# Kernel tuning notes

Measured on AMD Instinct MI355X. Metric: run time of the kernel, lower is better.

The kernel has to match this reference:

```python
import jax
jax.config.update("jax_enable_x64", True)
import jax.numpy as jnp
import numpy as np

SIGMA_2 = 0.1  # SNR = 10 dB -> sigma^2 = 1/10^(10/10)
P = 1.0        # total transmit power

NT, NR, DK, KU, BR = 64, 4, 2, 8, 16
BATCH = 256


def setup_inputs() -> dict:
    key = jax.random.key(0)
    k1, k2 = jax.random.split(key)
    channel = jax.random.normal(k1, (BATCH, NT * NR * BR * 2 * KU), dtype=jnp.float32)
    pred_w = 2 * NR * DK * KU * BR + DK * DK * KU * BR  # 2560
    prediction = jax.random.normal(k2, (BATCH, pred_w), dtype=jnp.float32)
    return {"channel": channel, "prediction": prediction,
            "Nt": NT, "Nr": NR, "dk": DK, "K": KU, "B": BR}


def reference(channel, prediction, Nt, Nr, dk, K, B):
    # --- unpack complex channel: [b, Nt, Nr, B, 2K] -> [b, Nr, Nt, B, K] complex
    Hc = channel.reshape(-1, Nt, Nr, B, 2 * K).astype(jnp.complex128)
    H = Hc[..., :K] + 1j * Hc[..., K:]
    H = jnp.transpose(H, (0, 2, 1, 3, 4))  # [b, Nr, Nt, B, K]

    nu = 2 * Nr * dk * K * B
    u_flat = prediction[:, :nu]
    w_flat = prediction[:, nu:nu + dk * dk * K * B]
    Uc = u_flat.reshape(-1, Nr, dk, B, 2 * K).astype(jnp.complex128)
    U = Uc[..., :K] + 1j * Uc[..., K:]           # [b, Nr, dk, B, K]
    W = w_flat.reshape(-1, dk, dk, B, K).astype(jnp.complex128)  # real-valued W

    # HHU[b,:,:,f,k] = H^H U  -> [b, Nt, dk, B, K]
    HHU = jnp.einsum('brtfk,brdfk->btdfk', jnp.conj(H), U)

    # sum over (rb, user) of sigma2/p * trace(U W U^H)
    tr_UWU = (SIGMA_2 / P) * jnp.einsum('brdfk,bdefk,brefk->b', U, W, jnp.conj(U))
    # sum over (rb, user) of (H^H U) W (H^H U)^H  -> [b, Nt, Nt]
    quad = jnp.einsum('btdfk,bdefk,bsefk->bts', HHU, W, jnp.conj(HHU))
    temp_B = quad + tr_UWU[:, None, None] * jnp.eye(Nt, dtype=jnp.complex128)
    temp_B_inv = jnp.linalg.inv(temp_B)  # batched Nt x Nt complex inverse

    # HUW[b,:,:,k] = sum_rb (H^H U) W  -> [b, Nt, dk, K]
    HUW = jnp.einsum('btdfk,bdefk->btek', HHU, W)
    V0 = jnp.einsum('bts,bsdk->btdk', temp_B_inv, HUW)  # [b, Nt, dk, K]

    # l2-normalize flattened precoder per sample (tf.linalg.normalize)
    flat = V0.reshape(-1, Nt * dk * K)
    flat = flat / jnp.linalg.norm(flat, axis=1, keepdims=True)
    V0 = flat.reshape(-1, Nt, dk, K)

    # power normalization: trace(sum_k V_k V_k^H)
    trace_VV = jnp.einsum('btdk,btdk->b', V0, jnp.conj(V0))
    scale = jnp.sqrt(P / jnp.real(trace_VV).astype(jnp.float32))
    V = V0 * scale.astype(jnp.complex128)[:, None, None, None]

    V = V.reshape(-1, Nt, dk, K, 1)
    return jnp.concatenate([jnp.real(V), jnp.imag(V)], axis=4).astype(jnp.float32)
```

## Files before the change

### kernel.cpp

```cpp
#include <hip/hip_runtime.h>
#include <math.h>


#define SAUG 84
#define STP  65

namespace {
union alignas(16) ShU {
    struct { float4 TtP[2][2][8][STP]; float4 HtP[2][2][8][STP]; } p1;
    float2 Aug[64][SAUG];
};
union alignas(16) ShV {
    struct { float2 U[4 * 258]; float W[512]; } in;
    float2 xout[64][17];
};
}

__device__ __forceinline__ float2 cmul(float2 x, float2 y) {
    return make_float2(x.x * y.x - x.y * y.y, x.x * y.y + x.y * y.x);
}

__global__ __launch_bounds__(512, 1)
void uw2v_kernel(const float* __restrict__ channel,
                 const float* __restrict__ prediction,
                 float2* __restrict__ out)
{
    __shared__ ShU sh;
    __shared__ ShV sv;
    __shared__ alignas(16) float2 prow[2][80];
    __shared__ float2 redbuf[8];
    __shared__ float  fred[8];

    const int b   = blockIdx.x;
    const int tid = threadIdx.x;
    const int wv  = tid >> 6;
    const float* pred = prediction + (size_t)b * 2560;
    const float* chan = channel + (size_t)b * 65536;

    #pragma unroll
    for (int i = 0; i < 2; ++i) {
        int m = tid + i * 512;
        int r = m >> 8, d = (m >> 7) & 1, f = (m >> 3) & 15, k = m & 7;
        const float* src = pred + (((r * 2 + d) * 16 + f) << 4);
        sv.in.U[r * 258 + ((d * 16 + f) << 3) + k] = make_float2(src[k], src[k + 8]);
    }
    sv.in.W[tid] = pred[2048 + tid];
    __syncthreads();

    const int half = tid >> 8;
    const int lt   = tid & 255;
    const int t4 = lt >> 2, r4 = lt & 3;
    const int a  = lt >> 4, bb = lt & 15;
    const int bit0 = r4 & 1, bit1 = (r4 >> 1) & 1;
    const int kkb  = 4 * bit0 + 2 * bit1;
    const int mpb  = kkb >> 1;
    const int fbase = half << 3;
    const int tr_r = lt >> 5, tr_d = (lt >> 4) & 1, tr_e = (lt >> 3) & 1, tr_k = lt & 7;

    float2 accA[4][4], accB[4][4];
    #pragma unroll
    for (int i = 0; i < 4; ++i)
        #pragma unroll
        for (int j = 0; j < 4; ++j) {
            accA[i][j] = make_float2(0.f, 0.f);
            accB[i][j] = make_float2(0.f, 0.f);
        }
    float2 huw[4] = {make_float2(0,0), make_float2(0,0), make_float2(0,0), make_float2(0,0)};
    float2 tracc  = make_float2(0.f, 0.f);

    const float* hbase = chan + ((t4 * 4 + r4) << 8) + (fbase << 4);

    #pragma unroll 1
    for (int fi = 0; fi < 8; ++fi) {
        const int f = fbase + fi;
        const float4 ca = *(const float4*)(hbase + (fi << 4) + 0);
        const float4 cb = *(const float4*)(hbase + (fi << 4) + 4);
        const float4 ci = *(const float4*)(hbase + (fi << 4) + 8);
        const float4 cd = *(const float4*)(hbase + (fi << 4) + 12);

        const float4* U0p = (const float4*)&sv.in.U[r4 * 258 + (f << 3)];
        const float4* U1p = (const float4*)&sv.in.U[r4 * 258 + ((16 + f) << 3)];
        const float4 u0q0 = U0p[0], u0q1 = U0p[1], u0q2 = U0p[2], u0q3 = U0p[3];
        const float4 u1q0 = U1p[0], u1q1 = U1p[1], u1q2 = U1p[2], u1q3 = U1p[3];

        float2 val0[8], val1[8];
        #define MK2(K, HR, HI, U0R, U0I, U1R, U1I) \
            val0[K] = make_float2((HR)*(U0R) + (HI)*(U0I), (HR)*(U0I) - (HI)*(U0R)); \
            val1[K] = make_float2((HR)*(U1R) + (HI)*(U1I), (HR)*(U1I) - (HI)*(U1R));
        MK2(0, ca.x, ci.x, u0q0.x, u0q0.y, u1q0.x, u1q0.y)
        MK2(1, ca.y, ci.y, u0q0.z, u0q0.w, u1q0.z, u1q0.w)
        MK2(2, ca.z, ci.z, u0q1.x, u0q1.y, u1q1.x, u1q1.y)
        MK2(3, ca.w, ci.w, u0q1.z, u0q1.w, u1q1.z, u1q1.w)
        MK2(4, cb.x, cd.x, u0q2.x, u0q2.y, u1q2.x, u1q2.y)
        MK2(5, cb.y, cd.y, u0q2.z, u0q2.w, u1q2.z, u1q2.w)
        MK2(6, cb.z, cd.z, u0q3.x, u0q3.y, u1q3.x, u1q3.y)
        MK2(7, cb.w, cd.w, u0q3.z, u0q3.w, u1q3.z, u1q3.w)
        #undef MK2

        float2 s1d0[4], s1d1[4];
        #pragma unroll
        for (int q = 0; q < 4; ++q) {
            float2 k0 = bit0 ? val0[4 + q] : val0[q];
            float2 n0 = bit0 ? val0[q]     : val0[4 + q];
            float2 k1 = bit0 ? val1[4 + q] : val1[q];
            float2 n1 = bit0 ? val1[q]     : val1[4 + q];
            n0.x = __shfl_xor(n0.x, 1); n0.y = __shfl_xor(n0.y, 1);
            n1.x = __shfl_xor(n1.x, 1); n1.y = __shfl_xor(n1.y, 1);
            s1d0[q] = make_float2(k0.x + n0.x, k0.y + n0.y);
            s1d1[q] = make_float2(k1.x + n1.x, k1.y + n1.y);
        }
        float2 h0[2], h1[2];
        #pragma unroll
        for (int jj = 0; jj < 2; ++jj) {
            float2 k0 = bit1 ? s1d0[2 + jj] : s1d0[jj];
            float2 n0 = bit1 ? s1d0[jj]     : s1d0[2 + jj];
            float2 k1 = bit1 ? s1d1[2 + jj] : s1d1[jj];
            float2 n1 = bit1 ? s1d1[jj]     : s1d1[2 + jj];
            n0.x = __shfl_xor(n0.x, 2); n0.y = __shfl_xor(n0.y, 2);
            n1.x = __shfl_xor(n1.x, 2); n1.y = __shfl_xor(n1.y, 2);
            h0[jj] = make_float2(k0.x + n0.x, k0.y + n0.y);
            h1[jj] = make_float2(k1.x + n1.x, k1.y + n1.y);
        }

        if (lt < 128) {
            float w   = sv.in.W[((tr_d * 2 + tr_e) * 16 + f) * 8 + tr_k];
            float2 u1 = sv.in.U[tr_r * 258 + ((tr_d * 16 + f) << 3) + tr_k];
            float2 u2 = sv.in.U[tr_r * 258 + ((tr_e * 16 + f) << 3) + tr_k];
            tracc.x += w * (u1.x * u2.x + u1.y * u2.y);
            tracc.y += w * (u1.y * u2.x - u1.x * u2.y);
        }

        const int p = fi & 1;
        #pragma unroll
        for (int e = 0; e < 2; ++e) {
            float w0a = sv.in.W[(e * 16 + f) * 8 + kkb];
            float w0b = sv.in.W[(e * 16 + f) * 8 + kkb + 1];
            float w1a = sv.in.W[((2 + e) * 16 + f) * 8 + kkb];
            float w1b = sv.in.W[((2 + e) * 16 + f) * 8 + kkb + 1];
            float2 tva = make_float2(h0[0].x * w0a + h1[0].x * w1a,
                                     h0[0].y * w0a + h1[0].y * w1a);
            float2 tvb = make_float2(h0[1].x * w0b + h1[1].x * w1b,
                                     h0[1].y * w0b + h1[1].y * w1b);
            sh.p1.TtP[p][half][e * 4 + mpb][t4] = make_float4(tva.x, tva.y, tvb.x, tvb.y);
            huw[e * 2 + 0].x += tva.x; huw[e * 2 + 0].y += tva.y;
            huw[e * 2 + 1].x += tvb.x; huw[e * 2 + 1].y += tvb.y;
        }
        sh.p1.HtP[p][half][mpb][t4]     = make_float4(h0[0].x, h0[0].y, h0[1].x, h0[1].y);
        sh.p1.HtP[p][half][4 + mpb][t4] = make_float4(h1[0].x, h1[0].y, h1[1].x, h1[1].y);
        __syncthreads();

        #pragma unroll
        for (int mp = 0; mp < 8; ++mp) {
            float4 tq[4], hq[4];
            #pragma unroll
            for (int i = 0; i < 4; ++i) tq[i] = sh.p1.TtP[p][half][mp][a + 16 * i];
            #pragma unroll
            for (int j = 0; j < 4; ++j) hq[j] = sh.p1.HtP[p][half][mp][bb + 16 * j];
            #pragma unroll
            for (int i = 0; i < 4; ++i)
                #pragma unroll
                for (int j = 0; j < 4; ++j) {
                    float2 va = accA[i][j], vb = accB[i][j];
                    va.x = fmaf(tq[i].x, hq[j].x, va.x);
                    va.y = fmaf(tq[i].x, hq[j].y, va.y);
                    vb.x = fmaf(tq[i].y, hq[j].x, vb.x);
                    vb.y = fmaf(tq[i].y, hq[j].y, vb.y);
                    va.x = fmaf(tq[i].z, hq[j].z, va.x);
                    va.y = fmaf(tq[i].z, hq[j].w, va.y);
                    vb.x = fmaf(tq[i].w, hq[j].z, vb.x);
                    vb.y = fmaf(tq[i].w, hq[j].w, vb.y);
                    accA[i][j] = va; accB[i][j] = vb;
                }
        }
    }

    #pragma unroll
    for (int off = 32; off; off >>= 1) {
        tracc.x += __shfl_xor(tracc.x, off);
        tracc.y += __shfl_xor(tracc.y, off);
    }
    if ((tid & 63) == 0) redbuf[wv] = tracc;
    __syncthreads();
    float2 trv = make_float2(0.f, 0.f);
    #pragma unroll
    for (int w = 0; w < 8; ++w) { trv.x += redbuf[w].x; trv.y += redbuf[w].y; }
    trv.x *= 0.1f; trv.y *= 0.1f;

    if (half == 0) {
        #pragma unroll
        for (int i = 0; i < 4; ++i)
            #pragma unroll
            for (int j = 0; j < 4; ++j) {
                float2 v = make_float2(accA[i][j].x + accB[i][j].y,
                                       accB[i][j].x - accA[i][j].y);
                int row = a + 16 * i, col = bb + 16 * j;
                if (row == col) { v.x += trv.x; v.y += trv.y; }
                sh.Aug[row][col] = v;
            }
        #pragma unroll
        for (int e = 0; e < 2; ++e)
            #pragma unroll
            for (int jj = 0; jj < 2; ++jj)
                sh.Aug[t4][64 + e * 8 + kkb + jj] = huw[e * 2 + jj];
    }
    __syncthreads();
    if (half == 1) {
        #pragma unroll
        for (int i = 0; i < 4; ++i)
            #pragma unroll
            for (int j = 0; j < 4; ++j) {
                int row = a + 16 * i, col = bb + 16 * j;
                float2 v = sh.Aug[row][col];
                v.x += accA[i][j].x + accB[i][j].y;
                v.y += accB[i][j].x - accA[i][j].y;
                sh.Aug[row][col] = v;
            }
        #pragma unroll
        for (int e = 0; e < 2; ++e)
            #pragma unroll
            for (int jj = 0; jj < 2; ++jj) {
                int col = 64 + e * 8 + kkb + jj;
                float2 v = sh.Aug[t4][col];
                v.x += huw[e * 2 + jj].x; v.y += huw[e * 2 + jj].y;
                sh.Aug[t4][col] = v;
            }
    }
    __syncthreads();

    const int gi = tid >> 3, gc = tid & 7;
    const int colbase = 10 * gc;
    const int lanebase = (tid & 63) & 56;

    float2 xr[10];
    {
        const float4* rp = (const float4*)&sh.Aug[gi][colbase];
        float4 q0 = rp[0], q1 = rp[1], q2 = rp[2], q3 = rp[3], q4 = rp[4];
        xr[0] = make_float2(q0.x, q0.y); xr[1] = make_float2(q0.z, q0.w);
        xr[2] = make_float2(q1.x, q1.y); xr[3] = make_float2(q1.z, q1.w);
        xr[4] = make_float2(q2.x, q2.y); xr[5] = make_float2(q2.z, q2.w);
        xr[6] = make_float2(q3.x, q3.y); xr[7] = make_float2(q3.z, q3.w);
        xr[8] = make_float2(q4.x, q4.y); xr[9] = make_float2(q4.z, q4.w);
    }
    if (gi == 0) {
        float4* wp = (float4*)&prow[0][colbase];
        wp[0] = make_float4(xr[0].x, xr[0].y, xr[1].x, xr[1].y);
        wp[1] = make_float4(xr[2].x, xr[2].y, xr[3].x, xr[3].y);
        wp[2] = make_float4(xr[4].x, xr[4].y, xr[5].x, xr[5].y);
        wp[3] = make_float4(xr[6].x, xr[6].y, xr[7].x, xr[7].y);
        wp[4] = make_float4(xr[8].x, xr[8].y, xr[9].x, xr[9].y);
    }
    __syncthreads();

    float2 myipv = make_float2(0.f, 0.f);

    #pragma unroll 1
    for (int ks = 0; ks < 64; ++ks) {
        const int pb = ks & 1;
        const float4* pp = (const float4*)&prow[pb][colbase];
        float4 p0 = pp[0], p1 = pp[1], p2 = pp[2], p3 = pp[3], p4 = pp[4];
        float2 pr[10];
        pr[0] = make_float2(p0.x, p0.y); pr[1] = make_float2(p0.z, p0.w);
        pr[2] = make_float2(p1.x, p1.y); pr[3] = make_float2(p1.z, p1.w);
        pr[4] = make_float2(p2.x, p2.y); pr[5] = make_float2(p2.z, p2.w);
        pr[6] = make_float2(p3.x, p3.y); pr[7] = make_float2(p3.z, p3.w);
        pr[8] = make_float2(p4.x, p4.y); pr[9] = make_float2(p4.z, p4.w);

        float2 z = prow[pb][ks];
        float  zi = 1.0f / (z.x * z.x + z.y * z.y);
        float2 ipv = make_float2(z.x * zi, -z.y * zi);

        float2 cand = make_float2(0.f, 0.f);
        #pragma unroll
        for (int c = 0; c < 10; ++c)
            if (colbase + c == ks) cand = xr[c];
        int srcl = lanebase + (ks / 10);
        float2 Lv;
        Lv.x = __shfl(cand.x, srcl);
        Lv.y = __shfl(cand.y, srcl);

        if (gi == ks) {
            myipv = ipv;
        } else {
            float2 L = cmul(Lv, ipv);
            #pragma unroll
            for (int c = 0; c < 10; ++c) {
                xr[c].x -= L.x * pr[c].x - L.y * pr[c].y;
                xr[c].y -= L.x * pr[c].y + L.y * pr[c].x;
            }
        }
        if (gi == ks + 1) {
            float4* wp = (float4*)&prow[pb ^ 1][colbase];
            wp[0] = make_float4(xr[0].x, xr[0].y, xr[1].x, xr[1].y);
            wp[1] = make_float4(xr[2].x, xr[2].y, xr[3].x, xr[3].y);
            wp[2] = make_float4(xr[4].x, xr[4].y, xr[5].x, xr[5].y);
            wp[3] = make_float4(xr[6].x, xr[6].y, xr[7].x, xr[7].y);
            wp[4] = make_float4(xr[8].x, xr[8].y, xr[9].x, xr[9].y);
        }
        __syncthreads();
    }

    float ss = 0.f;
    if (gc == 6) {
        #pragma unroll
        for (int c = 4; c < 10; ++c) {
            float2 xv = cmul(xr[c], myipv);
            ss += xv.x * xv.x + xv.y * xv.y;
            sv.xout[gi][c - 4] = xv;
        }
    } else if (gc == 7) {
        #pragma unroll
        for (int c = 0; c < 10; ++c) {
            float2 xv = cmul(xr[c], myipv);
            ss += xv.x * xv.x + xv.y * xv.y;
            sv.xout[gi][6 + c] = xv;
        }
    }
    #pragma unroll
    for (int off = 32; off; off >>= 1) ss += __shfl_xor(ss, off);
    if ((tid & 63) == 0) fred[wv] = ss;
    __syncthreads();
    float total = 0.f;
    #pragma unroll
    for (int w = 0; w < 8; ++w) total += fred[w];
    float invn = rsqrtf(total);
    #pragma unroll
    for (int q = 0; q < 2; ++q) {
        int m = tid + q * 512;
        float2 v = sv.xout[m >> 4][m & 15];
        out[(size_t)b * 1024 + m] = make_float2(v.x * invn, v.y * invn);
    }
}

extern "C" void kernel_launch(void* const* d_in, const int* in_sizes, int n_in,
                              void* d_out, int out_size, void* d_ws, size_t ws_size,
                              hipStream_t stream) {
    const float* channel    = (const float*)d_in[0];
    const float* prediction = (const float*)d_in[1];
    int batch = in_sizes[0] / 65536;
    uw2v_kernel<<<dim3(batch), dim3(512), 0, stream>>>(channel, prediction,
                                                       (float2*)d_out);
}
```

Baseline: 169.6 us.

## Double block to 1024 threads, split subcarriers across four groups

The block grows from 512 to 1024 threads. The Gram accumulation now splits the 16 resource blocks across four thread groups of 4 each instead of two groups of 8, which halves the serial loop length. The partial sums are reduced through two augmented shared matrices, and the diagonal regularizer is applied while summing them. The Gauss-Jordan elimination now gives each thread 5 columns instead of 10, which shortens the per-step work. The cost is doubled shared staging, more threads per block (which limits registers per thread), and 64 block-wide barriers over more waves.

```diff
diff --git a/kernel.cpp b/kernel.cpp
--- a/kernel.cpp
+++ b/kernel.cpp
@@ -7,8 +7,8 @@
 
 namespace {
 union alignas(16) ShU {
-    struct { float4 TtP[2][2][8][STP]; float4 HtP[2][2][8][STP]; } p1;
-    float2 Aug[64][SAUG];
+    struct { float4 TtP[2][4][8][STP]; float4 HtP[2][4][8][STP]; } p1;
+    struct { float2 A[64][SAUG]; float2 B[64][SAUG]; } aug;
 };
 union alignas(16) ShV {
     struct { float2 U[4 * 258]; float W[512]; } in;
@@ -20,7 +20,7 @@
     return make_float2(x.x * y.x - x.y * y.y, x.x * y.y + x.y * y.x);
 }
 
-__global__ __launch_bounds__(512, 1)
+__global__ __launch_bounds__(1024)
 void uw2v_kernel(const float* __restrict__ channel,
                  const float* __restrict__ prediction,
                  float2* __restrict__ out)
@@ -28,8 +28,8 @@
     __shared__ ShU sh;
     __shared__ ShV sv;
     __shared__ alignas(16) float2 prow[2][80];
-    __shared__ float2 redbuf[8];
-    __shared__ float  fred[8];
+    __shared__ float2 redbuf[16];
+    __shared__ float  fred[16];
 
     const int b   = blockIdx.x;
     const int tid = threadIdx.x;
@@ -37,24 +37,23 @@
     const float* pred = prediction + (size_t)b * 2560;
     const float* chan = channel + (size_t)b * 65536;
 
-    #pragma unroll
-    for (int i = 0; i < 2; ++i) {
-        int m = tid + i * 512;
+    {
+        int m = tid;
         int r = m >> 8, d = (m >> 7) & 1, f = (m >> 3) & 15, k = m & 7;
         const float* src = pred + (((r * 2 + d) * 16 + f) << 4);
         sv.in.U[r * 258 + ((d * 16 + f) << 3) + k] = make_float2(src[k], src[k + 8]);
     }
-    sv.in.W[tid] = pred[2048 + tid];
-    __syncthreads();
-
-    const int half = tid >> 8;
-    const int lt   = tid & 255;
+    if (tid < 512) sv.in.W[tid] = pred[2048 + tid];
+    __syncthreads();
+
+    const int grp = tid >> 8;
+    const int lt  = tid & 255;
     const int t4 = lt >> 2, r4 = lt & 3;
     const int a  = lt >> 4, bb = lt & 15;
     const int bit0 = r4 & 1, bit1 = (r4 >> 1) & 1;
     const int kkb  = 4 * bit0 + 2 * bit1;
     const int mpb  = kkb >> 1;
-    const int fbase = half << 3;
+    const int fbase = grp << 2;
     const int tr_r = lt >> 5, tr_d = (lt >> 4) & 1, tr_e = (lt >> 3) & 1, tr_k = lt & 7;
 
     float2 accA[4][4], accB[4][4];
@@ -71,7 +70,7 @@
     const float* hbase = chan + ((t4 * 4 + r4) << 8) + (fbase << 4);
 
     #pragma unroll 1
-    for (int fi = 0; fi < 8; ++fi) {
+    for (int fi = 0; fi < 4; ++fi) {
         const int f = fbase + fi;
         const float4 ca = *(const float4*)(hbase + (fi << 4) + 0);
         const float4 cb = *(const float4*)(hbase + (fi << 4) + 4);
@@ -141,21 +140,21 @@
                                      h0[0].y * w0a + h1[0].y * w1a);
             float2 tvb = make_float2(h0[1].x * w0b + h1[1].x * w1b,
                                      h0[1].y * w0b + h1[1].y * w1b);
-            sh.p1.TtP[p][half][e * 4 + mpb][t4] = make_float4(tva.x, tva.y, tvb.x, tvb.y);
+            sh.p1.TtP[p][grp][e * 4 + mpb][t4] = make_float4(tva.x, tva.y, tvb.x, tvb.y);
             huw[e * 2 + 0].x += tva.x; huw[e * 2 + 0].y += tva.y;
             huw[e * 2 + 1].x += tvb.x; huw[e * 2 + 1].y += tvb.y;
         }
-        sh.p1.HtP[p][half][mpb][t4]     = make_float4(h0[0].x, h0[0].y, h0[1].x, h0[1].y);
-        sh.p1.HtP[p][half][4 + mpb][t4] = make_float4(h1[0].x, h1[0].y, h1[1].x, h1[1].y);
+        sh.p1.HtP[p][grp][mpb][t4]     = make_float4(h0[0].x, h0[0].y, h0[1].x, h0[1].y);
+        sh.p1.HtP[p][grp][4 + mpb][t4] = make_float4(h1[0].x, h1[0].y, h1[1].x, h1[1].y);
         __syncthreads();
 
         #pragma unroll
         for (int mp = 0; mp < 8; ++mp) {
             float4 tq[4], hq[4];
             #pragma unroll
-            for (int i = 0; i < 4; ++i) tq[i] = sh.p1.TtP[p][half][mp][a + 16 * i];
-            #pragma unroll
-            for (int j = 0; j < 4; ++j) hq[j] = sh.p1.HtP[p][half][mp][bb + 16 * j];
+            for (int i = 0; i < 4; ++i) tq[i] = sh.p1.TtP[p][grp][mp][a + 16 * i];
+            #pragma unroll
+            for (int j = 0; j < 4; ++j) hq[j] = sh.p1.HtP[p][grp][mp][bb + 16 * j];
             #pragma unroll
             for (int i = 0; i < 4; ++i)
                 #pragma unroll
@@ -183,71 +182,65 @@
     __syncthreads();
     float2 trv = make_float2(0.f, 0.f);
     #pragma unroll
-    for (int w = 0; w < 8; ++w) { trv.x += redbuf[w].x; trv.y += redbuf[w].y; }
+    for (int w = 0; w < 16; ++w) { trv.x += redbuf[w].x; trv.y += redbuf[w].y; }
     trv.x *= 0.1f; trv.y *= 0.1f;
 
-    if (half == 0) {
+    if ((grp & 1) == 0) {
+        float2 (*Dst)[SAUG] = (grp == 0) ? sh.aug.A : sh.aug.B;
         #pragma unroll
         for (int i = 0; i < 4; ++i)
             #pragma unroll
             for (int j = 0; j < 4; ++j) {
-                float2 v = make_float2(accA[i][j].x + accB[i][j].y,
-                                       accB[i][j].x - accA[i][j].y);
-                int row = a + 16 * i, col = bb + 16 * j;
-                if (row == col) { v.x += trv.x; v.y += trv.y; }
-                sh.Aug[row][col] = v;
+                Dst[a + 16 * i][bb + 16 * j] =
+                    make_float2(accA[i][j].x + accB[i][j].y,
+                                accB[i][j].x - accA[i][j].y);
             }
         #pragma unroll
         for (int e = 0; e < 2; ++e)
             #pragma unroll
             for (int jj = 0; jj < 2; ++jj)
-                sh.Aug[t4][64 + e * 8 + kkb + jj] = huw[e * 2 + jj];
-    }
-    __syncthreads();
-    if (half == 1) {
+                Dst[t4][64 + e * 8 + kkb + jj] = huw[e * 2 + jj];
+    }
+    __syncthreads();
+    if (grp & 1) {
+        float2 (*Dst)[SAUG] = (grp == 1) ? sh.aug.A : sh.aug.B;
         #pragma unroll
         for (int i = 0; i < 4; ++i)
             #pragma unroll
             for (int j = 0; j < 4; ++j) {
-                int row = a + 16 * i, col = bb + 16 * j;
-                float2 v = sh.Aug[row][col];
+                float2 v = Dst[a + 16 * i][bb + 16 * j];
                 v.x += accA[i][j].x + accB[i][j].y;
                 v.y += accB[i][j].x - accA[i][j].y;
-                sh.Aug[row][col] = v;
+                Dst[a + 16 * i][bb + 16 * j] = v;
             }
         #pragma unroll
         for (int e = 0; e < 2; ++e)
             #pragma unroll
             for (int jj = 0; jj < 2; ++jj) {
                 int col = 64 + e * 8 + kkb + jj;
-                float2 v = sh.Aug[t4][col];
+                float2 v = Dst[t4][col];
                 v.x += huw[e * 2 + jj].x; v.y += huw[e * 2 + jj].y;
-                sh.Aug[t4][col] = v;
-            }
-    }
-    __syncthreads();
-
-    const int gi = tid >> 3, gc = tid & 7;
-    const int colbase = 10 * gc;
-    const int lanebase = (tid & 63) & 56;
-
-    float2 xr[10];
-    {
-        const float4* rp = (const float4*)&sh.Aug[gi][colbase];
-        float4 q0 = rp[0], q1 = rp[1], q2 = rp[2], q3 = rp[3], q4 = rp[4];
-        xr[0] = make_float2(q0.x, q0.y); xr[1] = make_float2(q0.z, q0.w);
-        xr[2] = make_float2(q1.x, q1.y); xr[3] = make_float2(q1.z, q1.w);
-        xr[4] = make_float2(q2.x, q2.y); xr[5] = make_float2(q2.z, q2.w);
-        xr[6] = make_float2(q3.x, q3.y); xr[7] = make_float2(q3.z, q3.w);
-        xr[8] = make_float2(q4.x, q4.y); xr[9] = make_float2(q4.z, q4.w);
+                Dst[t4][col] = v;
+            }
+    }
+    __syncthreads();
+
+    const int gi = tid >> 4, gc = tid & 15;
+    const int cb = gc * 5;
+    const int lanebase = (tid & 63) & 48;
+
+    float2 xr[5];
+    #pragma unroll
+    for (int c = 0; c < 5; ++c) {
+        float2 v = sh.aug.A[gi][cb + c];
+        float2 w = sh.aug.B[gi][cb + c];
+        v.x += w.x; v.y += w.y;
+        if (gi == cb + c) { v.x += trv.x; v.y += trv.y; }
+        xr[c] = v;
     }
     if (gi == 0) {
-        float4* wp = (float4*)&prow[0][colbase];
-        wp[0] = make_float4(xr[0].x, xr[0].y, xr[1].x, xr[1].y);
-        wp[1] = make_float4(xr[2].x, xr[2].y, xr[3].x, xr[3].y);
-        wp[2] = make_float4(xr[4].x, xr[4].y, xr[5].x, xr[5].y);
-        wp[3] = make_float4(xr[6].x, xr[6].y, xr[7].x, xr[7].y);
-        wp[4] = make_float4(xr[8].x, xr[8].y, xr[9].x, xr[9].y);
+        #pragma unroll
+        for (int c = 0; c < 5; ++c) prow[0][cb + c] = xr[c];
     }
     __syncthreads();
 
@@ -256,14 +249,9 @@
     #pragma unroll 1
     for (int ks = 0; ks < 64; ++ks) {
         const int pb = ks & 1;
-        const float4* pp = (const float4*)&prow[pb][colbase];
-        float4 p0 = pp[0], p1 = pp[1], p2 = pp[2], p3 = pp[3], p4 = pp[4];
-        float2 pr[10];
-        pr[0] = make_float2(p0.x, p0.y); pr[1] = make_float2(p0.z, p0.w);
-        pr[2] = make_float2(p1.x, p1.y); pr[3] = make_float2(p1.z, p1.w);
-        pr[4] = make_float2(p2.x, p2.y); pr[5] = make_float2(p2.z, p2.w);
-        pr[6] = make_float2(p3.x, p3.y); pr[7] = make_float2(p3.z, p3.w);
-        pr[8] = make_float2(p4.x, p4.y); pr[9] = make_float2(p4.z, p4.w);
+        float2 pr[5];
+        #pragma unroll
+        for (int c = 0; c < 5; ++c) pr[c] = prow[pb][cb + c];
 
         float2 z = prow[pb][ks];
         float  zi = 1.0f / (z.x * z.x + z.y * z.y);
@@ -271,9 +259,9 @@
 
         float2 cand = make_float2(0.f, 0.f);
         #pragma unroll
-        for (int c = 0; c < 10; ++c)
-            if (colbase + c == ks) cand = xr[c];
-        int srcl = lanebase + (ks / 10);
+        for (int c = 0; c < 5; ++c)
+            if (cb + c == ks) cand = xr[c];
+        int srcl = lanebase + (ks / 5);
         float2 Lv;
         Lv.x = __shfl(cand.x, srcl);
         Lv.y = __shfl(cand.y, srcl);
@@ -283,36 +271,28 @@
         } else {
             float2 L = cmul(Lv, ipv);
             #pragma unroll
-            for (int c = 0; c < 10; ++c) {
+            for (int c = 0; c < 5; ++c) {
                 xr[c].x -= L.x * pr[c].x - L.y * pr[c].y;
                 xr[c].y -= L.x * pr[c].y + L.y * pr[c].x;
             }
         }
         if (gi == ks + 1) {
-            float4* wp = (float4*)&prow[pb ^ 1][colbase];
-            wp[0] = make_float4(xr[0].x, xr[0].y, xr[1].x, xr[1].y);
-            wp[1] = make_float4(xr[2].x, xr[2].y, xr[3].x, xr[3].y);
-            wp[2] = make_float4(xr[4].x, xr[4].y, xr[5].x, xr[5].y);
-            wp[3] = make_float4(xr[6].x, xr[6].y, xr[7].x, xr[7].y);
-            wp[4] = make_float4(xr[8].x, xr[8].y, xr[9].x, xr[9].y);
+            #pragma unroll
+            for (int c = 0; c < 5; ++c) prow[pb ^ 1][cb + c] = xr[c];
         }
         __syncthreads();
     }
 
     float ss = 0.f;
-    if (gc == 6) {
-        #pragma unroll
-        for (int c = 4; c < 10; ++c) {
-            float2 xv = cmul(xr[c], myipv);
-            ss += xv.x * xv.x + xv.y * xv.y;
-            sv.xout[gi][c - 4] = xv;
-        }
-    } else if (gc == 7) {
-        #pragma unroll
-        for (int c = 0; c < 10; ++c) {
-            float2 xv = cmul(xr[c], myipv);
-            ss += xv.x * xv.x + xv.y * xv.y;
-            sv.xout[gi][6 + c] = xv;
+    if (gc >= 12) {
+        #pragma unroll
+        for (int c = 0; c < 5; ++c) {
+            int col = cb + c;
+            if (col >= 64) {
+                float2 xv = cmul(xr[c], myipv);
+                ss += xv.x * xv.x + xv.y * xv.y;
+                sv.xout[gi][col - 64] = xv;
+            }
         }
     }
     #pragma unroll
@@ -321,13 +301,11 @@
     __syncthreads();
     float total = 0.f;
     #pragma unroll
-    for (int w = 0; w < 8; ++w) total += fred[w];
+    for (int w = 0; w < 16; ++w) total += fred[w];
     float invn = rsqrtf(total);
-    #pragma unroll
-    for (int q = 0; q < 2; ++q) {
-        int m = tid + q * 512;
-        float2 v = sv.xout[m >> 4][m & 15];
-        out[(size_t)b * 1024 + m] = make_float2(v.x * invn, v.y * invn);
+    {
+        float2 v = sv.xout[tid >> 4][tid & 15];
+        out[(size_t)b * 1024 + tid] = make_float2(v.x * invn, v.y * invn);
     }
 }
 
@@ -337,6 +315,6 @@
     const float* channel    = (const float*)d_in[0];
     const float* prediction = (const float*)d_in[1];
     int batch = in_sizes[0] / 65536;
-    uw2v_kernel<<<dim3(batch), dim3(512), 0, stream>>>(channel, prediction,
-                                                       (float2*)d_out);
+    uw2v_kernel<<<dim3(batch), dim3(1024), 0, stream>>>(channel, prediction,
+                                                        (float2*)d_out);
 }
```

After: 249.7 us. +47.2%, slower.

## Block Gauss-Jordan elimination into 8-row panels with in-wave cascade and shuffles

Applied to the files above, without the earlier changes.

Restructures the 64-step Gauss-Jordan inversion so each wave holds 8 pivot rows and eliminates them internally with warp shuffles. The other waves then apply the whole panel of 8 pivots read from shared memory. This cuts the block-wide barriers from 64 to about 9 and overlaps the next panel's cascade with the current elimination. The cost is extra shuffle traffic and serialized per-wave cascade work, which sits on the critical path.

```diff
diff --git a/kernel.cpp b/kernel.cpp
--- a/kernel.cpp
+++ b/kernel.cpp
@@ -27,7 +27,8 @@
 {
     __shared__ ShU sh;
     __shared__ ShV sv;
-    __shared__ alignas(16) float2 prow[2][80];
+    __shared__ alignas(16) float2 pivR[2][8][80];
+    __shared__ float2 pivI[2][8];
     __shared__ float2 redbuf[8];
     __shared__ float  fred[8];
 
@@ -228,12 +229,12 @@
     __syncthreads();
 
     const int gi = tid >> 3, gc = tid & 7;
-    const int colbase = 10 * gc;
+    const int cb = 10 * gc;
     const int lanebase = (tid & 63) & 56;
 
     float2 xr[10];
     {
-        const float4* rp = (const float4*)&sh.Aug[gi][colbase];
+        const float4* rp = (const float4*)&sh.Aug[gi][cb];
         float4 q0 = rp[0], q1 = rp[1], q2 = rp[2], q3 = rp[3], q4 = rp[4];
         xr[0] = make_float2(q0.x, q0.y); xr[1] = make_float2(q0.z, q0.w);
         xr[2] = make_float2(q1.x, q1.y); xr[3] = make_float2(q1.z, q1.w);
@@ -241,62 +242,93 @@
         xr[6] = make_float2(q3.x, q3.y); xr[7] = make_float2(q3.z, q3.w);
         xr[8] = make_float2(q4.x, q4.y); xr[9] = make_float2(q4.z, q4.w);
     }
-    if (gi == 0) {
-        float4* wp = (float4*)&prow[0][colbase];
+
+    float2 myipv = make_float2(0.f, 0.f);
+
+    auto cascade = [&](int chunk, int nb) {
+        #pragma unroll
+        for (int p = 0; p < 8; ++p) {
+            const int col = 8 * chunk + p;
+            const int cs  = col / 10;
+            float2 cand = make_float2(0.f, 0.f);
+            #pragma unroll
+            for (int c = 0; c < 10; ++c)
+                if (cb + c == col) cand = xr[c];
+            float2 z, Lv;
+            z.x  = __shfl(cand.x, p * 8 + cs);
+            z.y  = __shfl(cand.y, p * 8 + cs);
+            Lv.x = __shfl(cand.x, lanebase + cs);
+            Lv.y = __shfl(cand.y, lanebase + cs);
+            float  zi  = 1.0f / (z.x * z.x + z.y * z.y);
+            float2 ipv = make_float2(z.x * zi, -z.y * zi);
+            const bool isPiv = (gi == col);
+            if (isPiv) myipv = ipv;
+            float2 pr[10];
+            #pragma unroll
+            for (int c = 0; c < 10; ++c) {
+                pr[c].x = __shfl(xr[c].x, p * 8 + gc);
+                pr[c].y = __shfl(xr[c].y, p * 8 + gc);
+            }
+            if (!isPiv) {
+                float2 L = cmul(Lv, ipv);
+                #pragma unroll
+                for (int c = 0; c < 10; ++c) {
+                    xr[c].x -= L.x * pr[c].x - L.y * pr[c].y;
+                    xr[c].y -= L.x * pr[c].y + L.y * pr[c].x;
+                }
+            }
+        }
+        const int prw = gi & 7;
+        float4* wp = (float4*)&pivR[nb][prw][cb];
         wp[0] = make_float4(xr[0].x, xr[0].y, xr[1].x, xr[1].y);
         wp[1] = make_float4(xr[2].x, xr[2].y, xr[3].x, xr[3].y);
         wp[2] = make_float4(xr[4].x, xr[4].y, xr[5].x, xr[5].y);
         wp[3] = make_float4(xr[6].x, xr[6].y, xr[7].x, xr[7].y);
         wp[4] = make_float4(xr[8].x, xr[8].y, xr[9].x, xr[9].y);
-    }
-    __syncthreads();
-
-    float2 myipv = make_float2(0.f, 0.f);
-
-    #pragma unroll 1
-    for (int ks = 0; ks < 64; ++ks) {
-        const int pb = ks & 1;
-        const float4* pp = (const float4*)&prow[pb][colbase];
-        float4 p0 = pp[0], p1 = pp[1], p2 = pp[2], p3 = pp[3], p4 = pp[4];
-        float2 pr[10];
-        pr[0] = make_float2(p0.x, p0.y); pr[1] = make_float2(p0.z, p0.w);
-        pr[2] = make_float2(p1.x, p1.y); pr[3] = make_float2(p1.z, p1.w);
-        pr[4] = make_float2(p2.x, p2.y); pr[5] = make_float2(p2.z, p2.w);
-        pr[6] = make_float2(p3.x, p3.y); pr[7] = make_float2(p3.z, p3.w);
-        pr[8] = make_float2(p4.x, p4.y); pr[9] = make_float2(p4.z, p4.w);
-
-        float2 z = prow[pb][ks];
-        float  zi = 1.0f / (z.x * z.x + z.y * z.y);
-        float2 ipv = make_float2(z.x * zi, -z.y * zi);
-
-        float2 cand = make_float2(0.f, 0.f);
-        #pragma unroll
-        for (int c = 0; c < 10; ++c)
-            if (colbase + c == ks) cand = xr[c];
-        int srcl = lanebase + (ks / 10);
-        float2 Lv;
-        Lv.x = __shfl(cand.x, srcl);
-        Lv.y = __shfl(cand.y, srcl);
-
-        if (gi == ks) {
-            myipv = ipv;
-        } else {
+        if (gc == 0) pivI[nb][prw] = myipv;
+    };
+
+    auto eliminate = [&](int chunk, int bf) {
+        #pragma unroll
+        for (int p = 0; p < 8; ++p) {
+            const int col = 8 * chunk + p;
+            float2 cand = make_float2(0.f, 0.f);
+            #pragma unroll
+            for (int c = 0; c < 10; ++c)
+                if (cb + c == col) cand = xr[c];
+            float2 Lv;
+            Lv.x = __shfl(cand.x, lanebase + col / 10);
+            Lv.y = __shfl(cand.y, lanebase + col / 10);
+            float2 ipv = pivI[bf][p];
             float2 L = cmul(Lv, ipv);
+            const float4* pp = (const float4*)&pivR[bf][p][cb];
+            float4 p0 = pp[0], p1 = pp[1], p2 = pp[2], p3 = pp[3], p4 = pp[4];
+            float2 pr[10];
+            pr[0] = make_float2(p0.x, p0.y); pr[1] = make_float2(p0.z, p0.w);
+            pr[2] = make_float2(p1.x, p1.y); pr[3] = make_float2(p1.z, p1.w);
+            pr[4] = make_float2(p2.x, p2.y); pr[5] = make_float2(p2.z, p2.w);
+            pr[6] = make_float2(p3.x, p3.y); pr[7] = make_float2(p3.z, p3.w);
+            pr[8] = make_float2(p4.x, p4.y); pr[9] = make_float2(p4.z, p4.w);
             #pragma unroll
             for (int c = 0; c < 10; ++c) {
                 xr[c].x -= L.x * pr[c].x - L.y * pr[c].y;
                 xr[c].y -= L.x * pr[c].y + L.y * pr[c].x;
             }
         }
-        if (gi == ks + 1) {
-            float4* wp = (float4*)&prow[pb ^ 1][colbase];
-            wp[0] = make_float4(xr[0].x, xr[0].y, xr[1].x, xr[1].y);
-            wp[1] = make_float4(xr[2].x, xr[2].y, xr[3].x, xr[3].y);
-            wp[2] = make_float4(xr[4].x, xr[4].y, xr[5].x, xr[5].y);
-            wp[3] = make_float4(xr[6].x, xr[6].y, xr[7].x, xr[7].y);
-            wp[4] = make_float4(xr[8].x, xr[8].y, xr[9].x, xr[9].y);
+    };
+
+    int cur = 0;
+    if (wv == 0) cascade(0, 0);
+    __syncthreads();
+
+    #pragma unroll 1
+    for (int c = 0; c < 8; ++c) {
+        if (wv != c) {
+            eliminate(c, cur);
+            if (wv == c + 1) cascade(c + 1, cur ^ 1);
         }
         __syncthreads();
+        cur ^= 1;
     }
 
     float ss = 0.f;
```

Result: faster. 166.2 us (-2.1%).
